# Performance work log

Measured on AMD Instinct MI355X. Metric: run time of the kernel, lower is better.

The kernel has to match this reference:

```python
import jax, jax.numpy as jnp
import numpy as np

NC = 65536   # candidate centers across FPN levels (single image)
NP = 1024    # proposal boxes == points
D = 256      # points_feat_dim
C = 256      # in_channels (query/key dim)
START_LEVEL = 3
NEG = -1e30


def setup_inputs() -> dict:
    key = jax.random.key(0)
    ks = jax.random.split(key, 9)
    # centers: [y, x, size, stride]; stride in {8,16,32,64,128} -> lvl 0..4
    lvl = jax.random.randint(ks[0], (NC,), 0, 5)
    stride = (2.0 ** (lvl + START_LEVEL)).astype(jnp.float32)
    yx = jax.random.uniform(ks[1], (NC, 2), minval=0.0, maxval=1024.0)
    centers = jnp.concatenate([yx, stride[:, None], stride[:, None]], axis=1)
    # boxes: [x1, y1, x2, y2]
    x1y1 = jax.random.uniform(ks[2], (NP, 2), minval=0.0, maxval=900.0)
    wh = jax.random.uniform(ks[3], (NP, 2), minval=64.0, maxval=256.0)
    boxes = jnp.concatenate([x1y1, x1y1 + wh], axis=1)
    points_feat = jax.random.normal(ks[4], (NP, D), dtype=jnp.float32)
    box_feat = jax.random.normal(ks[5], (NC, D), dtype=jnp.float32)
    Wq = jax.random.normal(ks[6], (D, C), dtype=jnp.float32) / np.sqrt(D).astype(np.float32)
    bq = jnp.zeros((C,), dtype=jnp.float32)
    Wk = jax.random.normal(ks[7], (D, C), dtype=jnp.float32) / np.sqrt(D).astype(np.float32)
    bk = jnp.zeros((C,), dtype=jnp.float32)
    scales = 1.0 + 0.1 * jax.random.normal(ks[8], (5,), dtype=jnp.float32)
    return dict(points_feat=points_feat, box_feat=box_feat, centers=centers,
                boxes=boxes, Wq=Wq, bq=bq, Wk=Wk, bk=bk, scales=scales)


def reference(points_feat, box_feat, centers, boxes, Wq, bq, Wk, bk, scales):
    # geometry -> containment mask [NC, NP] (center c inside box p)
    coord = centers[:, :2] + jnp.floor_divide(centers[:, 2:3], 2.0)  # [NC,2]
    ys, xs = coord[:, 0], coord[:, 1]
    l = xs[:, None] - boxes[None, :, 0]
    t = ys[:, None] - boxes[None, :, 1]
    r = boxes[None, :, 2] - xs[:, None]
    b = boxes[None, :, 3] - ys[:, None]
    mask = jnp.minimum(jnp.minimum(l, t), jnp.minimum(r, b)) > 0     # [NC,NP]

    stride = centers[:, 3]
    lvl = (jnp.log2(stride) - START_LEVEL).astype(jnp.int32)         # [NC] in 0..4
    w = scales[lvl]                                                  # per-level scale

    query = points_feat @ Wq + bq                                    # [NP,C]
    keyf = (box_feat * w[:, None]) @ Wk + bk                         # [NC,C]

    sim = jnp.clip(keyf @ query.T, -50.0, 50.0)                      # [NC,NP]
    logits = jnp.where(mask, sim, NEG)
    attn = jax.nn.softmax(logits, axis=0)
    attn = jnp.where(mask, attn, 0.0)                                # zero out invalid
    merge = attn.T @ box_feat                                        # [NP,D]
    return points_feat + merge
```

## Files before the change

kernel.cpp:

```cpp
#include <hip/hip_runtime.h>

typedef unsigned short ushort_t;
typedef _Float16 half8 __attribute__((ext_vector_type(8)));
typedef short short8 __attribute__((ext_vector_type(8)));
typedef float floatx4 __attribute__((ext_vector_type(4)));

#define NCC 65536
#define NPP 1024
#define DD 256
#define NCHUNK 64
#define VROW 36
#define VTILE_B (256 * VROW * 2)

static __device__ __forceinline__ ushort_t f2h_bits(float x) {
  _Float16 h = (_Float16)x;
  return __builtin_bit_cast(ushort_t, h);
}
static __device__ __forceinline__ ushort_t f2bf_bits(float x) {
  unsigned u = __builtin_bit_cast(unsigned, x);
  unsigned r = (u + 0x7FFFu + ((u >> 16) & 1u)) >> 16;
  return (ushort_t)r;
}

static __device__ __forceinline__ void dma16(const void* g, void* l) {
  __builtin_amdgcn_global_load_lds((const __attribute__((address_space(1))) unsigned int*)g,
                                   (__attribute__((address_space(3))) unsigned int*)l, 16, 0, 0);
}

static __device__ __forceinline__ short8 mk_s8(uint2 lo, uint2 hi) {
  uint4 u;
  u.x = lo.x; u.y = lo.y; u.z = hi.x; u.w = hi.y;
  return __builtin_bit_cast(short8, u);
}

__global__ __launch_bounds__(256) void wt_prep(const float* __restrict__ Wq,
                                               const float* __restrict__ Wk,
                                               ushort_t* __restrict__ WqT,
                                               ushort_t* __restrict__ WkT) {
  __shared__ __align__(16) ushort_t lt[64][80];
  const float* W = blockIdx.y ? Wk : Wq;
  ushort_t* WT = blockIdx.y ? WkT : WqT;
  const int k0 = ((int)blockIdx.x & 3) * 64, n0 = ((int)blockIdx.x >> 2) * 64;
  const int t = threadIdx.x;
#pragma unroll
  for (int i = 0; i < 4; i++) {
    int f = t + 256 * i;
    int k = f >> 4, j = (f & 15) * 4;
    const float4 v = *(const float4*)&W[(size_t)(k0 + k) * DD + n0 + j];
    lt[j + 0][k] = f2h_bits(v.x);
    lt[j + 1][k] = f2h_bits(v.y);
    lt[j + 2][k] = f2h_bits(v.z);
    lt[j + 3][k] = f2h_bits(v.w);
  }
  __syncthreads();
#pragma unroll
  for (int i = 0; i < 2; i++) {
    int f = t + 256 * i;
    int nl = f >> 3, grp = f & 7;
    int n = n0 + nl;
    int kp = k0 + ((grp ^ (n & 7)) * 8);
    *(uint4*)&WT[(size_t)n * DD + kp] = *(const uint4*)&lt[nl][grp * 8];
  }
}

__global__ __launch_bounds__(256) void prep_gemm(
    const float* __restrict__ box_feat, const float* __restrict__ points_feat,
    const float* __restrict__ centers, const float* __restrict__ scales,
    const ushort_t* __restrict__ WqT, const ushort_t* __restrict__ WkT,
    const float* __restrict__ bq, const float* __restrict__ bk,
    ushort_t* __restrict__ q_out, ushort_t* __restrict__ kf_out,
    float2* __restrict__ xy) {
  __shared__ __align__(16) ushort_t lds_a[64][264];
  __shared__ __align__(16) ushort_t lds_b[64 * 256];
  __shared__ __align__(16) ushort_t lds_o[64][72];
  __shared__ float lds_s[64];

  const int t = threadIdx.x;
  const bool isQ = (blockIdx.x >= (NCC / 64));
  const int row0 = isQ ? ((int)blockIdx.x - NCC / 64) * 64 : (int)blockIdx.x * 64;
  const float* In = isQ ? points_feat : box_feat;
  const ushort_t* WT = isQ ? WqT : WkT;
  const float* Bi = isQ ? bq : bk;
  ushort_t* Out = isQ ? q_out : kf_out;
  const int swz = isQ ? 0 : 7;

  if (t < 64) {
    float s = 1.0f;
    if (!isQ) {
      int c = row0 + t;
      float stride = centers[c * 4 + 3];
      int lvl = (int)(log2f(stride) + 0.5f) - 3;
      lvl = lvl < 0 ? 0 : (lvl > 4 ? 4 : lvl);
      s = scales[lvl];
      float hf = floorf(centers[c * 4 + 2] * 0.5f);
      xy[c] = make_float2(centers[c * 4 + 1] + hf, centers[c * 4 + 0] + hf);
    }
    lds_s[t] = s;
  }
  __syncthreads();

#pragma unroll
  for (int i = 0; i < 16; i++) {
    int f = t + 256 * i;
    int r = f >> 6;
    int c4 = (f & 63) * 4;
    const float4 v = *(const float4*)&In[(size_t)(row0 + r) * DD + c4];
    float s = lds_s[r];
    ushort_t h0 = f2h_bits(v.x * s), h1 = f2h_bits(v.y * s);
    ushort_t h2 = f2h_bits(v.z * s), h3 = f2h_bits(v.w * s);
    *(uint2*)&lds_a[r][c4] =
        make_uint2((unsigned)h0 | ((unsigned)h1 << 16), (unsigned)h2 | ((unsigned)h3 << 16));
  }

  const int w = t >> 6, lane = t & 63, qd = lane >> 4, n = lane & 15;
  const int sw8 = (n & 7) * 8;

  for (int g = 0; g < 4; ++g) {
    __syncthreads();
#pragma unroll
    for (int j = 0; j < 8; ++j) {
      int sg = w * 8 + j;
      dma16(&WT[(size_t)g * 64 * DD + sg * 512 + lane * 8], &lds_b[sg * 512 + lane * 8]);
    }
    __syncthreads();

    floatx4 acc[4] = {};
#pragma unroll
    for (int s = 0; s < 8; s++) {
      half8 af = __builtin_bit_cast(half8, *(const uint4*)&lds_a[w * 16 + n][s * 32 + qd * 8]);
      int off = (s * 32 + qd * 8) ^ sw8;
#pragma unroll
      for (int nt = 0; nt < 4; ++nt) {
        half8 bf = __builtin_bit_cast(half8, *(const uint4*)&lds_b[(nt * 16 + n) * 256 + off]);
        acc[nt] = __builtin_amdgcn_mfma_f32_16x16x32_f16(af, bf, acc[nt], 0, 0, 0);
      }
    }
#pragma unroll
    for (int nt = 0; nt < 4; ++nt) {
      float b = Bi[g * 64 + nt * 16 + n];
#pragma unroll
      for (int r = 0; r < 4; r++) lds_o[w * 16 + qd * 4 + r][nt * 16 + n] = f2h_bits(acc[nt][r] + b);
    }
    __syncthreads();
#pragma unroll
    for (int i = 0; i < 2; i++) {
      int idx = t * 2 + i;
      int r = idx >> 3, grp = idx & 7;
      uint4 v = *(const uint4*)&lds_o[r][grp * 8];
      int grpS = grp ^ (swz & (r & 7));
      *(uint4*)&Out[(size_t)(row0 + r) * DD + (g * 8 + grpS) * 8] = v;
    }
  }
}

__global__ __launch_bounds__(256) void transpose_v(const float* __restrict__ box_feat,
                                                   ushort_t* __restrict__ vTb) {
  __shared__ __align__(16) ushort_t lt[64][72];
  const int t = threadIdx.x;
  const int c0 = blockIdx.x * 64, d0 = blockIdx.y * 64;
#pragma unroll
  for (int i = 0; i < 4; i++) {
    int f = t + 256 * i;
    int c = f >> 4;
    int j = (f & 15) * 4;
    const float4 v = *(const float4*)&box_feat[(size_t)(c0 + c) * DD + d0 + j];
    lt[j + 0][c] = f2bf_bits(v.x);
    lt[j + 1][c] = f2bf_bits(v.y);
    lt[j + 2][c] = f2bf_bits(v.z);
    lt[j + 3][c] = f2bf_bits(v.w);
  }
  __syncthreads();
#pragma unroll
  for (int i = 0; i < 2; i++) {
    int f = t + 256 * i;
    int d = f >> 3, j = f & 7;
    int tile = (c0 >> 5) + (j >> 2);
    size_t ob = (size_t)tile * (256 * VROW) + (size_t)(d0 + d) * VROW + (j & 3) * 8;
    const uint2* src = (const uint2*)&lt[d][j * 8];
    *(uint2*)&vTb[ob] = src[0];
    *(uint2*)&vTb[ob + 4] = src[1];
  }
}

template <bool PART>
__global__ __launch_bounds__(256, 2) void attn_kernel(
    const ushort_t* __restrict__ qf16, const ushort_t* __restrict__ kf16,
    const ushort_t* __restrict__ vTb, const float2* __restrict__ xy,
    const float* __restrict__ boxes, float* __restrict__ acc_out,
    float* __restrict__ den_out) {
  __shared__ __align__(16) ushort_t lds_k[2][32 * 256];
  __shared__ __align__(16) ushort_t lds_v[2][256 * VROW];
  __shared__ __align__(16) ushort_t lds_p[4][32][VROW];

  const int t = threadIdx.x;
  const int w = t >> 6, lane = t & 63, qd = lane >> 4, n = lane & 15;
  const int chunk = blockIdx.x;
  const int p0w = blockIdx.y * 128 + w * 32;
  const int cchunk = chunk * 1024;
  const int sw16 = (n & 7) * 16;

  half8 qfr[2][8];
  float4 bxv[2];
#pragma unroll
  for (int pt = 0; pt < 2; ++pt) {
    int p = p0w + pt * 16 + n;
#pragma unroll
    for (int s = 0; s < 8; s++)
      qfr[pt][s] =
          __builtin_bit_cast(half8, *(const uint4*)&qf16[(size_t)p * DD + s * 32 + qd * 8]);
    bxv[pt] = *(const float4*)&boxes[p * 4];
  }

  floatx4 macc[2][16] = {};
  float dsum0 = 0.f, dsum1 = 0.f;

  auto stage = [&](int it, int buf) {
    const size_t kbase = (size_t)(cchunk + it * 32) * DD * 2;
#pragma unroll
    for (int j = 0; j < 4; ++j) {
      int i = w * 4 + j;
      dma16((const char*)kf16 + kbase + i * 1024 + lane * 16,
            (char*)lds_k[buf] + i * 1024 + lane * 16);
    }
    const size_t vbase = (size_t)((cchunk >> 5) + it) * VTILE_B;
#pragma unroll
    for (int j = 0; j < 4; ++j) {
      int i = j * 4 + w;
      dma16((const char*)vTb + vbase + i * 1024 + lane * 16,
            (char*)lds_v[buf] + i * 1024 + lane * 16);
    }
    if (w < 2) {
      int i = 16 + w;
      dma16((const char*)vTb + vbase + i * 1024 + lane * 16,
            (char*)lds_v[buf] + i * 1024 + lane * 16);
    }
  };

  stage(0, 0);

  for (int it = 0; it < 32; ++it) {
    const int buf = it & 1;
    const int cb = cchunk + it * 32;
    __syncthreads();
    if (it + 1 < 32) stage(it + 1, buf ^ 1);

#pragma unroll
    for (int t2 = 0; t2 < 2; ++t2) {
      const char* krow = (const char*)lds_k[buf] + (t2 * 16 + n) * 512;
      floatx4 a0 = {}, a1 = {};
#pragma unroll
      for (int s = 0; s < 8; s++) {
        half8 af = __builtin_bit_cast(half8, *(const uint4*)(krow + ((s * 64 + qd * 16) ^ sw16)));
        a0 = __builtin_amdgcn_mfma_f32_16x16x32_f16(af, qfr[0][s], a0, 0, 0, 0);
        a1 = __builtin_amdgcn_mfma_f32_16x16x32_f16(af, qfr[1][s], a1, 0, 0, 0);
      }
      unsigned pk00 = 0, pk01 = 0, pk10 = 0, pk11 = 0;
#pragma unroll
      for (int r = 0; r < 4; r++) {
        int cl = t2 * 16 + qd * 4 + r;
        float2 pxy = xy[cb + cl];
        {
          float mn = fminf(fminf(pxy.x - bxv[0].x, pxy.y - bxv[0].y),
                           fminf(bxv[0].z - pxy.x, bxv[0].w - pxy.y));
          float sim = fminf(fmaxf(a0[r], -50.f), 50.f);
          float e = (mn > 0.f) ? exp2f((sim - 50.f) * 1.44269504f) : 0.f;
          dsum0 += e;
          unsigned b = (unsigned)f2bf_bits(e);
          if (r == 0) pk00 = b;
          else if (r == 1) pk00 |= b << 16;
          else if (r == 2) pk01 = b;
          else pk01 |= b << 16;
        }
        {
          float mn = fminf(fminf(pxy.x - bxv[1].x, pxy.y - bxv[1].y),
                           fminf(bxv[1].z - pxy.x, bxv[1].w - pxy.y));
          float sim = fminf(fmaxf(a1[r], -50.f), 50.f);
          float e = (mn > 0.f) ? exp2f((sim - 50.f) * 1.44269504f) : 0.f;
          dsum1 += e;
          unsigned b = (unsigned)f2bf_bits(e);
          if (r == 0) pk10 = b;
          else if (r == 1) pk10 |= b << 16;
          else if (r == 2) pk11 = b;
          else pk11 |= b << 16;
        }
      }
      *(uint2*)&lds_p[w][n][t2 * 16 + qd * 4] = make_uint2(pk00, pk01);
      *(uint2*)&lds_p[w][16 + n][t2 * 16 + qd * 4] = make_uint2(pk10, pk11);
    }
    __asm__ volatile("s_waitcnt lgkmcnt(0)" ::: "memory");

    const char* pr0 = (const char*)&lds_p[w][n][0];
    const char* pr1 = (const char*)&lds_p[w][16 + n][0];
    short8 a20 = mk_s8(*(const uint2*)(pr0 + qd * 16), *(const uint2*)(pr0 + qd * 16 + 8));
    short8 a21 = mk_s8(*(const uint2*)(pr1 + qd * 16), *(const uint2*)(pr1 + qd * 16 + 8));
#pragma unroll
    for (int dt = 0; dt < 16; ++dt) {
      const char* vrow = (const char*)lds_v[buf] + (dt * 16 + n) * (VROW * 2);
      short8 b2 = mk_s8(*(const uint2*)(vrow + qd * 16), *(const uint2*)(vrow + qd * 16 + 8));
      macc[0][dt] = __builtin_amdgcn_mfma_f32_16x16x32_bf16(a20, b2, macc[0][dt], 0, 0, 0);
      macc[1][dt] = __builtin_amdgcn_mfma_f32_16x16x32_bf16(a21, b2, macc[1][dt], 0, 0, 0);
    }
  }

  dsum0 += __shfl_xor(dsum0, 16, 64);
  dsum0 += __shfl_xor(dsum0, 32, 64);
  dsum1 += __shfl_xor(dsum1, 16, 64);
  dsum1 += __shfl_xor(dsum1, 32, 64);

  if (PART) {
    if (lane < 16) {
      den_out[(size_t)chunk * NPP + p0w + n] = dsum0;
      den_out[(size_t)chunk * NPP + p0w + 16 + n] = dsum1;
    }
    float* ab = acc_out + (size_t)chunk * NPP * DD;
#pragma unroll
    for (int pt = 0; pt < 2; ++pt)
#pragma unroll
      for (int dt = 0; dt < 16; ++dt)
#pragma unroll
        for (int r = 0; r < 4; r++)
          ab[(size_t)(p0w + pt * 16 + qd * 4 + r) * DD + dt * 16 + n] = macc[pt][dt][r];
  } else {
    if (lane < 16) {
      atomicAdd(&den_out[p0w + n], dsum0);
      atomicAdd(&den_out[p0w + 16 + n], dsum1);
    }
#pragma unroll
    for (int pt = 0; pt < 2; ++pt)
#pragma unroll
      for (int dt = 0; dt < 16; ++dt)
#pragma unroll
        for (int r = 0; r < 4; r++)
          atomicAdd(&acc_out[(size_t)(p0w + pt * 16 + qd * 4 + r) * DD + dt * 16 + n],
                    macc[pt][dt][r]);
  }
}

__global__ __launch_bounds__(256) void reduce_finalize(const float* __restrict__ points_feat,
                                                       const float* __restrict__ acc_part,
                                                       const float* __restrict__ den_part,
                                                       float* __restrict__ out) {
  const int p = blockIdx.x, t = threadIdx.x;
  float s = 0.f;
#pragma unroll 4
  for (int c = 0; c < NCHUNK; ++c) s += acc_part[((size_t)c * NPP + p) * DD + t];
  float dn = den_part[(size_t)(t & 63) * NPP + p];
#pragma unroll
  for (int o = 1; o < 64; o <<= 1) dn += __shfl_xor(dn, o, 64);
  float m = (dn > 0.f) ? s / dn : 0.f;
  out[(size_t)p * DD + t] = points_feat[(size_t)p * DD + t] + m;
}

__global__ void finalize(const float* __restrict__ points_feat, const float* __restrict__ acc,
                         const float* __restrict__ den, float* __restrict__ out) {
  int p = blockIdx.x, d = threadIdx.x;
  float dn = den[p];
  float m = (dn > 0.f) ? acc[p * DD + d] / dn : 0.f;
  out[p * DD + d] = points_feat[p * DD + d] + m;
}

extern "C" void kernel_launch(void* const* d_in, const int* in_sizes, int n_in, void* d_out,
                              int out_size, void* d_ws, size_t ws_size, hipStream_t stream) {
  const float* points_feat = (const float*)d_in[0];
  const float* box_feat = (const float*)d_in[1];
  const float* centers = (const float*)d_in[2];
  const float* boxes = (const float*)d_in[3];
  const float* Wq = (const float*)d_in[4];
  const float* bq = (const float*)d_in[5];
  const float* Wk = (const float*)d_in[6];
  const float* bk = (const float*)d_in[7];
  const float* scales = (const float*)d_in[8];

  char* p = (char*)d_ws;
  ushort_t* ws_q = (ushort_t*)p;        p += (size_t)NPP * DD * 2;
  ushort_t* ws_kf = (ushort_t*)p;       p += (size_t)NCC * DD * 2;
  ushort_t* ws_vTb = (ushort_t*)p;      p += (size_t)(NCC / 32) * VTILE_B;
  float2* ws_xy = (float2*)p;           p += (size_t)NCC * 8;
  ushort_t* ws_wqT = (ushort_t*)p;      p += (size_t)DD * DD * 2;
  ushort_t* ws_wkT = (ushort_t*)p;      p += (size_t)DD * DD * 2;
  float* ws_den = (float*)p;            p += (size_t)NCHUNK * NPP * 4;
  float* ws_acc = (float*)p;
  size_t need_part = (size_t)(p - (char*)d_ws) + (size_t)NCHUNK * NPP * DD * 4;
  const bool part = ws_size >= need_part;

  wt_prep<<<dim3(16, 2), 256, 0, stream>>>(Wq, Wk, ws_wqT, ws_wkT);
  prep_gemm<<<NCC / 64 + NPP / 64, 256, 0, stream>>>(box_feat, points_feat, centers, scales,
                                                     ws_wqT, ws_wkT, bq, bk, ws_q, ws_kf, ws_xy);
  transpose_v<<<dim3(NCC / 64, DD / 64), 256, 0, stream>>>(box_feat, ws_vTb);
  if (part) {
    attn_kernel<true><<<dim3(NCHUNK, 8), 256, 0, stream>>>(ws_q, ws_kf, ws_vTb, ws_xy, boxes,
                                                           ws_acc, ws_den);
    reduce_finalize<<<NPP, 256, 0, stream>>>(points_feat, ws_acc, ws_den, (float*)d_out);
  } else {
    hipMemsetAsync(ws_den, 0, ((size_t)NPP * DD + NPP) * sizeof(float), stream);
    float* acc1 = ws_den + NPP;
    attn_kernel<false><<<dim3(NCHUNK, 8), 256, 0, stream>>>(ws_q, ws_kf, ws_vTb, ws_xy, boxes,
                                                            acc1, ws_den);
    finalize<<<NPP, DD, 0, stream>>>(points_feat, acc1, ws_den, (float*)d_out);
  }
}
```

Before: 282.1 us.

## Transpose softmax probabilities in registers with permlane swaps instead of LDS

```diff
diff --git a/kernel.cpp b/kernel.cpp
--- a/kernel.cpp
+++ b/kernel.cpp
@@ -31,6 +31,18 @@
   uint4 u;
   u.x = lo.x; u.y = lo.y; u.z = hi.x; u.w = hi.y;
   return __builtin_bit_cast(short8, u);
+}
+
+static __device__ __forceinline__ unsigned cvt_pk_bf16(float lo, float hi) {
+  unsigned r;
+  asm("v_cvt_pk_bf16_f32 %0, %1, %2" : "=v"(r) : "v"(lo), "v"(hi));
+  return r;
+}
+static __device__ __forceinline__ void swap32(unsigned& a, unsigned& b) {
+  asm("v_permlane32_swap_b32 %0, %1" : "+v"(a), "+v"(b));
+}
+static __device__ __forceinline__ void swap16(unsigned& a, unsigned& b) {
+  asm("v_permlane16_swap_b32 %0, %1" : "+v"(a), "+v"(b));
 }
 
 __global__ __launch_bounds__(256) void wt_prep(const float* __restrict__ Wq,
@@ -190,7 +202,6 @@
     float* __restrict__ den_out) {
   __shared__ __align__(16) ushort_t lds_k[2][32 * 256];
   __shared__ __align__(16) ushort_t lds_v[2][256 * VROW];
-  __shared__ __align__(16) ushort_t lds_p[4][32][VROW];
 
   const int t = threadIdx.x;
   const int w = t >> 6, lane = t & 63, qd = lane >> 4, n = lane & 15;
@@ -244,6 +255,7 @@
     __syncthreads();
     if (it + 1 < 32) stage(it + 1, buf ^ 1);
 
+    unsigned pkA[2][2], pkB[2][2];
 #pragma unroll
     for (int t2 = 0; t2 < 2; ++t2) {
       const char* krow = (const char*)lds_k[buf] + (t2 * 16 + n) * 512;
@@ -254,45 +266,50 @@
         a0 = __builtin_amdgcn_mfma_f32_16x16x32_f16(af, qfr[0][s], a0, 0, 0, 0);
         a1 = __builtin_amdgcn_mfma_f32_16x16x32_f16(af, qfr[1][s], a1, 0, 0, 0);
       }
-      unsigned pk00 = 0, pk01 = 0, pk10 = 0, pk11 = 0;
+      float ev0[4], ev1[4];
 #pragma unroll
       for (int r = 0; r < 4; r++) {
         int cl = t2 * 16 + qd * 4 + r;
         float2 pxy = xy[cb + cl];
         {
-          float mn = fminf(fminf(pxy.x - bxv[0].x, pxy.y - bxv[0].y),
-                           fminf(bxv[0].z - pxy.x, bxv[0].w - pxy.y));
-          float sim = fminf(fmaxf(a0[r], -50.f), 50.f);
-          float e = (mn > 0.f) ? exp2f((sim - 50.f) * 1.44269504f) : 0.f;
+          int m = (pxy.x > bxv[0].x) & (pxy.y > bxv[0].y) &
+                  (pxy.x < bxv[0].z) & (pxy.y < bxv[0].w);
+          float sim = __builtin_amdgcn_fmed3f(a0[r], -50.f, 50.f);
+          float e = m ? exp2f(__builtin_fmaf(sim, 1.44269504f, -72.1347520444f)) : 0.f;
           dsum0 += e;
-          unsigned b = (unsigned)f2bf_bits(e);
-          if (r == 0) pk00 = b;
-          else if (r == 1) pk00 |= b << 16;
-          else if (r == 2) pk01 = b;
-          else pk01 |= b << 16;
+          ev0[r] = e;
         }
         {
-          float mn = fminf(fminf(pxy.x - bxv[1].x, pxy.y - bxv[1].y),
-                           fminf(bxv[1].z - pxy.x, bxv[1].w - pxy.y));
-          float sim = fminf(fmaxf(a1[r], -50.f), 50.f);
-          float e = (mn > 0.f) ? exp2f((sim - 50.f) * 1.44269504f) : 0.f;
+          int m = (pxy.x > bxv[1].x) & (pxy.y > bxv[1].y) &
+                  (pxy.x < bxv[1].z) & (pxy.y < bxv[1].w);
+          float sim = __builtin_amdgcn_fmed3f(a1[r], -50.f, 50.f);
+          float e = m ? exp2f(__builtin_fmaf(sim, 1.44269504f, -72.1347520444f)) : 0.f;
           dsum1 += e;
-          unsigned b = (unsigned)f2bf_bits(e);
-          if (r == 0) pk10 = b;
-          else if (r == 1) pk10 |= b << 16;
-          else if (r == 2) pk11 = b;
-          else pk11 |= b << 16;
+          ev1[r] = e;
         }
       }
-      *(uint2*)&lds_p[w][n][t2 * 16 + qd * 4] = make_uint2(pk00, pk01);
-      *(uint2*)&lds_p[w][16 + n][t2 * 16 + qd * 4] = make_uint2(pk10, pk11);
-    }
-    __asm__ volatile("s_waitcnt lgkmcnt(0)" ::: "memory");
-
-    const char* pr0 = (const char*)&lds_p[w][n][0];
-    const char* pr1 = (const char*)&lds_p[w][16 + n][0];
-    short8 a20 = mk_s8(*(const uint2*)(pr0 + qd * 16), *(const uint2*)(pr0 + qd * 16 + 8));
-    short8 a21 = mk_s8(*(const uint2*)(pr1 + qd * 16), *(const uint2*)(pr1 + qd * 16 + 8));
+      pkA[t2][0] = cvt_pk_bf16(ev0[0], ev0[1]);
+      pkA[t2][1] = cvt_pk_bf16(ev0[2], ev0[3]);
+      pkB[t2][0] = cvt_pk_bf16(ev1[0], ev1[1]);
+      pkB[t2][1] = cvt_pk_bf16(ev1[2], ev1[3]);
+    }
+    unsigned A0 = pkA[0][0], B0 = pkA[0][1], C0 = pkA[1][0], D0 = pkA[1][1];
+    swap32(A0, C0);
+    swap32(B0, D0);
+    swap16(A0, C0);
+    swap16(B0, D0);
+    unsigned A1 = pkB[0][0], B1 = pkB[0][1], C1 = pkB[1][0], D1 = pkB[1][1];
+    swap32(A1, C1);
+    swap32(B1, D1);
+    swap16(A1, C1);
+    swap16(B1, D1);
+    uint4 u0;
+    u0.x = A0; u0.y = B0; u0.z = C0; u0.w = D0;
+    uint4 u1;
+    u1.x = A1; u1.y = B1; u1.z = C1; u1.w = D1;
+    short8 a20 = __builtin_bit_cast(short8, u0);
+    short8 a21 = __builtin_bit_cast(short8, u1);
+
 #pragma unroll
     for (int dt = 0; dt < 16; ++dt) {
       const char* vrow = (const char*)lds_v[buf] + (dt * 16 + n) * (VROW * 2);
```

After: 420.1 us. 48.9% more time.
